# Kernel tuning notes

Measured on AMD Instinct MI355X. Metric: run time of the kernel, lower is better.

The kernel has to match this reference:

```python
import jax, jax.numpy as jnp
import numpy as np

B, S, HID = 1, 2048, 4096
H, HKV, D = 32, 8, 128
GROUPS = H // HKV
ROPE_BASE = 10000.0


def setup_inputs() -> dict:
    key = jax.random.key(0)
    k1, k2, k3, k4, k5 = jax.random.split(key, 5)
    s = 0.02
    return {
        "hidden_states": jax.random.normal(k1, (B, S, HID), dtype=jnp.float32),
        "Wq": jax.random.normal(k2, (H * D, HID), dtype=jnp.float32) * s,
        "Wk": jax.random.normal(k3, (HKV * D, HID), dtype=jnp.float32) * s,
        "Wv": jax.random.normal(k4, (HKV * D, HID), dtype=jnp.float32) * s,
        "Wo": jax.random.normal(k5, (HID, H * D), dtype=jnp.float32) * s,
    }


def _rotate_half(x):
    x1, x2 = x[..., : D // 2], x[..., D // 2 :]
    return jnp.concatenate((-x2, x1), axis=-1)


def _rope_tables(seq_len):
    inv_freq = 1.0 / (ROPE_BASE ** (jnp.arange(0, D, 2, dtype=jnp.float32) / D))
    t = jnp.arange(seq_len, dtype=jnp.float32)
    freqs = jnp.outer(t, inv_freq)            # [S, D/2]
    emb = jnp.concatenate((freqs, freqs), -1)  # [S, D]
    return jnp.cos(emb)[None, None], jnp.sin(emb)[None, None]  # [1,1,S,D]


def reference(hidden_states, Wq, Wk, Wv, Wo):
    b, s, _ = hidden_states.shape
    scale = D ** -0.5
    q = (hidden_states @ Wq.T).reshape(b, s, H, D).transpose(0, 2, 1, 3)    # [B,H,S,D]
    k = (hidden_states @ Wk.T).reshape(b, s, HKV, D).transpose(0, 2, 1, 3)  # [B,HKV,S,D]
    v = (hidden_states @ Wv.T).reshape(b, s, HKV, D).transpose(0, 2, 1, 3)

    cos, sin = _rope_tables(s)
    q = q * cos + _rotate_half(q) * sin
    k = k * cos + _rotate_half(k) * sin

    # repeat_kv: h = kv_h * groups + g -> consecutive repeat along head axis
    k_rep = jnp.repeat(k, GROUPS, axis=1)  # [B,H,S,D]
    v_rep = jnp.repeat(v, GROUPS, axis=1)

    scores = jnp.einsum("bhqd,bhkd->bhqk", q, k_rep) * scale
    causal = jnp.tril(jnp.ones((s, s), dtype=bool))
    scores = jnp.where(causal[None, None], scores, jnp.finfo(scores.dtype).min)
    probs = jax.nn.softmax(scores, axis=-1)
    attn = jnp.einsum("bhqk,bhkd->bhqd", probs, v_rep)  # [B,H,S,D]
    attn = attn.transpose(0, 2, 1, 3).reshape(b, s, H * D)
    return attn @ Wo.T
```

## Files before the change

### kernel.cpp

```cpp
#include <hip/hip_runtime.h>

#define AS1 __attribute__((address_space(1)))
#define AS3 __attribute__((address_space(3)))

typedef __bf16 bf16;
typedef __bf16 bf16x8 __attribute__((ext_vector_type(8)));
typedef float f32x4 __attribute__((ext_vector_type(4)));

__device__ __forceinline__ void gld_lds16(const bf16* g, bf16* l) {
    __builtin_amdgcn_global_load_lds((const AS1 void*)g, (AS3 void*)l, 16, 0, 0);
}

#define SB0 __builtin_amdgcn_sched_barrier(0)
#define BARX do { SB0; __builtin_amdgcn_s_barrier(); SB0; } while (0)

__global__ void cvt_all_kernel(const float4* __restrict__ h, const float4* __restrict__ wq,
                               const float4* __restrict__ wk, const float4* __restrict__ wv,
                               const float4* __restrict__ wo, ushort4* __restrict__ hs,
                               ushort4* __restrict__ wb) {
    const int i = blockIdx.x * 256 + threadIdx.x;
    const float4* src;
    ushort4* dst;
    if (i < 2097152)      { src = h  + i;             dst = hs + i; }
    else if (i < 6291456) { src = wq + (i - 2097152); dst = wb + (i - 2097152); }
    else if (i < 7340032) { src = wk + (i - 6291456); dst = wb + 4194304 + (i - 6291456); }
    else if (i < 8388608) { src = wv + (i - 7340032); dst = wb + 5242880 + (i - 7340032); }
    else                  { src = wo + (i - 8388608); dst = wb + 6291456 + (i - 8388608); }
    const float4 v = *src;
    ushort4 r;
    r.x = __builtin_bit_cast(unsigned short, (bf16)v.x);
    r.y = __builtin_bit_cast(unsigned short, (bf16)v.y);
    r.z = __builtin_bit_cast(unsigned short, (bf16)v.z);
    r.w = __builtin_bit_cast(unsigned short, (bf16)v.w);
    *dst = r;
}

template <bool OUTF32>
__launch_bounds__(512, 2)
__global__ void gemm_8ph_kernel(const bf16* __restrict__ A, const bf16* __restrict__ W,
                                void* __restrict__ Cout, int M, int N, int K) {
    __shared__ __align__(16) bf16 Asl[2][256 * 64];
    __shared__ __align__(16) bf16 Bsl[2][256 * 64];

    const int tn = blockIdx.x * 256;
    const int tm = blockIdx.y * 256;
    const int tid = threadIdx.x;
    const int wave = tid >> 6;
    const int lane = tid & 63;
    const int laneR = lane & 15;
    const int laneS = lane >> 4;
    const int wmB = (wave >> 2) * 128;
    const int wnB = (wave & 3) * 64;
    const int NT = K >> 6;
    const int NI = NT >> 1;

    auto stageA = [&](int t, int h) {
        if (t >= NT) return;
        const int d = t & 1, k0 = t << 6;
#pragma unroll
        for (int iss = 0; iss < 2; ++iss) {
            const int c = iss * 512 + tid;
            const int row = c >> 3, sl = c & 7;
            gld_lds16(A + (size_t)(tm + h * 128 + row) * K + k0 + ((sl ^ (row & 7)) << 3),
                      &Asl[d][h * 8192 + (iss * 512 + wave * 64) * 8]);
        }
    };
    auto stageB = [&](int t, int h) {
        if (t >= NT) return;
        const int d = t & 1, k0 = t << 6;
#pragma unroll
        for (int iss = 0; iss < 2; ++iss) {
            const int c = iss * 512 + tid;
            const int row = c >> 3, sl = c & 7;
            gld_lds16(W + (size_t)(tn + h * 128 + row) * K + k0 + ((sl ^ (row & 7)) << 3),
                      &Bsl[d][h * 8192 + (iss * 512 + wave * 64) * 8]);
        }
    };

    bf16x8 aF[8], bF0[4], bF1[4];
    f32x4 acc[8][4] = {};

#define RD_A(d, mh) do { _Pragma("unroll") for (int m = 0; m < 4; ++m) \
    _Pragma("unroll") for (int ks = 0; ks < 2; ++ks) { \
        const int row_ = wmB + (mh) * 64 + m * 16 + laneR; \
        const int sl_ = (ks * 4 + laneS) ^ (row_ & 7); \
        aF[m * 2 + ks] = *(const bf16x8*)&Asl[d][row_ * 64 + sl_ * 8]; } } while (0)

#define RD_B(d, nh, DST) do { _Pragma("unroll") for (int n = 0; n < 2; ++n) \
    _Pragma("unroll") for (int ks = 0; ks < 2; ++ks) { \
        const int row_ = wnB + (nh) * 32 + n * 16 + laneR; \
        const int sl_ = (ks * 4 + laneS) ^ (row_ & 7); \
        DST[n * 2 + ks] = *(const bf16x8*)&Bsl[d][row_ * 64 + sl_ * 8]; } } while (0)

#define MMAQ(mh, nh, BSRC) do { __builtin_amdgcn_s_setprio(1); \
    _Pragma("unroll") for (int m = 0; m < 4; ++m) \
    _Pragma("unroll") for (int n = 0; n < 2; ++n) \
    _Pragma("unroll") for (int ks = 0; ks < 2; ++ks) \
        acc[(mh) * 4 + m][(nh) * 2 + n] = __builtin_amdgcn_mfma_f32_16x16x32_bf16( \
            aF[m * 2 + ks], BSRC[n * 2 + ks], acc[(mh) * 4 + m][(nh) * 2 + n], 0, 0, 0); \
    __builtin_amdgcn_s_setprio(0); } while (0)

    stageA(0, 0); stageA(0, 1); stageB(0, 0); stageB(0, 1); stageA(1, 0);
    SB0; asm volatile("s_waitcnt vmcnt(2)" ::: "memory"); BARX;

    for (int i = 0; i < NI; ++i) {
        const int u = i * 2;
        const bool last = (i == NI - 1);
        RD_A(0, 0); RD_B(0, 0, bF0); stageA(u + 1, 1);
        BARX; MMAQ(0, 0, bF0); BARX;
        RD_B(0, 1, bF1); stageB(u + 1, 0);
        BARX; MMAQ(0, 1, bF1); BARX;
        RD_A(0, 1); stageB(u + 1, 1);
        BARX; MMAQ(1, 1, bF1); BARX;
        RD_B(0, 0, bF0); stageA(u + 2, 0);
        BARX; MMAQ(1, 0, bF0);
        SB0;
        if (last) asm volatile("s_waitcnt vmcnt(0)" ::: "memory");
        else      asm volatile("s_waitcnt vmcnt(2)" ::: "memory");
        BARX;
        RD_A(1, 0); RD_B(1, 0, bF0); stageA(u + 2, 1);
        BARX; MMAQ(0, 0, bF0); BARX;
        RD_B(1, 1, bF1); stageB(u + 2, 0);
        BARX; MMAQ(0, 1, bF1); BARX;
        RD_A(1, 1); stageB(u + 2, 1);
        BARX; MMAQ(1, 1, bF1); BARX;
        RD_B(1, 0, bF0); stageA(u + 3, 0);
        BARX; MMAQ(1, 0, bF0);
        SB0;
        if (last) asm volatile("s_waitcnt vmcnt(0)" ::: "memory");
        else      asm volatile("s_waitcnt vmcnt(2)" ::: "memory");
        BARX;
    }
#undef RD_A
#undef RD_B
#undef MMAQ

    const int rbase = laneS * 4;
#pragma unroll
    for (int mf = 0; mf < 8; ++mf)
#pragma unroll
        for (int nf = 0; nf < 4; ++nf)
#pragma unroll
            for (int rr = 0; rr < 4; ++rr) {
                const size_t row = (size_t)tm + wmB + mf * 16 + rbase + rr;
                const size_t col = (size_t)tn + wnB + nf * 16 + laneR;
                if constexpr (OUTF32) ((float*)Cout)[row * N + col] = acc[mf][nf][rr];
                else                  ((bf16*)Cout)[row * N + col] = (bf16)acc[mf][nf][rr];
            }
    (void)M;
}

template <int BN, bool OUTF32>
__launch_bounds__(512, 2)
__global__ void gemm8p_kernel(const bf16* __restrict__ A, const bf16* __restrict__ W,
                              void* __restrict__ Cout, int M, int N, int K) {
    constexpr int NF = BN / 64;
    constexpr int IB = BN / 128;
    __shared__ __align__(16) bf16 Asl[4][128 * 32];
    __shared__ __align__(16) bf16 Bsl[4][BN * 32];

    const int tn = blockIdx.x * BN;
    const int tm = blockIdx.y * 128;
    const int tid = threadIdx.x;
    const int wave = tid >> 6;
    const int lane = tid & 63;
    const int laneR = lane & 15;
    const int laneS = lane >> 4;
    const int wmB = (wave >> 2) * 64;
    const int wnB = (wave & 3) * (BN / 4);
    const int NT = K >> 5;
    const int sofs = (laneS ^ ((laneR >> 1) & 3)) << 3;

    auto stage = [&](int t) {
        const int slot = t & 3;
        const int k0 = t << 5;
        {
            const int row = tid >> 2, g = tid & 3;
            const int sg = g ^ ((row >> 1) & 3);
            gld_lds16(A + (size_t)(tm + row) * K + k0 + sg * 8, &Asl[slot][wave * 512]);
        }
#pragma unroll
        for (int i = 0; i < IB; ++i) {
            const int row = i * 128 + (tid >> 2), g = tid & 3;
            const int sg = g ^ ((row >> 1) & 3);
            gld_lds16(W + (size_t)(tn + row) * K + k0 + sg * 8,
                      &Bsl[slot][i * 4096 + wave * 512]);
        }
    };

    f32x4 acc[4][NF] = {};

    stage(0); stage(1); stage(2);
    asm volatile("s_waitcnt vmcnt(6)" ::: "memory");
    SB0;
    __builtin_amdgcn_s_barrier();
    SB0;

    for (int t = 0; t < NT; ++t) {
        const int slot = t & 3;
        bf16x8 af[4], bfr[NF];
#pragma unroll
        for (int mf = 0; mf < 4; ++mf)
            af[mf] = *(const bf16x8*)&Asl[slot][(wmB + mf * 16 + laneR) * 32 + sofs];
#pragma unroll
        for (int nf = 0; nf < NF; ++nf)
            bfr[nf] = *(const bf16x8*)&Bsl[slot][(wnB + nf * 16 + laneR) * 32 + sofs];

        if (t + 3 < NT) stage(t + 3);

#pragma unroll
        for (int mf = 0; mf < 4; ++mf)
#pragma unroll
            for (int nf = 0; nf < NF; ++nf)
                acc[mf][nf] = __builtin_amdgcn_mfma_f32_16x16x32_bf16(af[mf], bfr[nf], acc[mf][nf], 0, 0, 0);

        SB0;
        if (t + 3 < NT)       asm volatile("s_waitcnt vmcnt(6)" ::: "memory");
        else if (t + 3 == NT) asm volatile("s_waitcnt vmcnt(3)" ::: "memory");
        else                  asm volatile("s_waitcnt vmcnt(0)" ::: "memory");
        SB0;
        __builtin_amdgcn_s_barrier();
        SB0;
    }

    const int rbase = laneS * 4;
#pragma unroll
    for (int mf = 0; mf < 4; ++mf)
#pragma unroll
        for (int nf = 0; nf < NF; ++nf)
#pragma unroll
            for (int rr = 0; rr < 4; ++rr) {
                const size_t row = (size_t)tm + wmB + mf * 16 + rbase + rr;
                const size_t col = (size_t)tn + wnB + nf * 16 + laneR;
                if constexpr (OUTF32) ((float*)Cout)[row * N + col] = acc[mf][nf][rr];
                else                  ((bf16*)Cout)[row * N + col] = (bf16)acc[mf][nf][rr];
            }
    (void)M;
}

__global__ void rope_table_kernel(float* __restrict__ ct, float* __restrict__ st) {
    const int idx = blockIdx.x * 256 + threadIdx.x;
    const int f = idx & 63;
    const int s = idx >> 6;
    const float th = s * expf(-0.14391156831212787f * (float)f);
    ct[idx] = cosf(th);
    st[idx] = sinf(th);
}

__global__ void rope_qk_kernel(const bf16* __restrict__ C, bf16* __restrict__ Qr, bf16* __restrict__ Kr,
                               const float* __restrict__ ct, const float* __restrict__ st) {
    const int idx = blockIdx.x * 256 + threadIdx.x;
    const int NQ = 2048 * 32 * 64;
    const float QSC = 0.12751743561884394f;
    if (idx < NQ) {
        const int f = idx & 63;
        const int t = idx >> 6;
        const int h = t & 31;
        const int s = t >> 5;
        const float x1 = (float)C[(size_t)s * 6144 + h * 128 + f];
        const float x2 = (float)C[(size_t)s * 6144 + h * 128 + f + 64];
        const float cs = ct[(s << 6) + f], sn = st[(s << 6) + f];
        bf16* dst = Qr + ((size_t)h * 2048 + s) * 128 + f;
        dst[0]  = (bf16)((x1 * cs - x2 * sn) * QSC);
        dst[64] = (bf16)((x2 * cs + x1 * sn) * QSC);
    } else {
        const int i2 = idx - NQ;
        const int f = i2 & 63;
        const int t = i2 >> 6;
        const int h = t & 7;
        const int s = t >> 3;
        const float x1 = (float)C[(size_t)s * 6144 + 4096 + h * 128 + f];
        const float x2 = (float)C[(size_t)s * 6144 + 4096 + h * 128 + f + 64];
        const float cs = ct[(s << 6) + f], sn = st[(s << 6) + f];
        bf16* dst = Kr + ((size_t)h * 2048 + s) * 128 + f;
        dst[0]  = (bf16)(x1 * cs - x2 * sn);
        dst[64] = (bf16)(x2 * cs + x1 * sn);
    }
}

__global__ void transpose_v_kernel(const bf16* __restrict__ C, bf16* __restrict__ Vt) {
    __shared__ __align__(16) unsigned short t[64][136];
    const int hkv = blockIdx.x >> 5;
    const int st = blockIdx.x & 31;
    const int s0 = st * 64;
    const int tid = threadIdx.x;
#pragma unroll
    for (int it = 0; it < 4; ++it) {
        const int l = it * 2048 + tid * 8;
        const int r = l >> 7, c = l & 127;
        *(bf16x8*)&t[r][c] = *(const bf16x8*)&C[(size_t)(s0 + r) * 6144 + 5120 + hkv * 128 + c];
    }
    __syncthreads();
#pragma unroll
    for (int it = 0; it < 8; ++it) {
        const int o = it * 1024 + tid * 4;
        const int d = o >> 6, j = o & 63;
        ushort4 pk;
        pk.x = t[j + 0][d];
        pk.y = t[j + 1][d];
        pk.z = t[j + 2][d];
        pk.w = t[j + 3][d];
        *(ushort4*)&Vt[((size_t)hkv * 128 + d) * 2048 + s0 + j] = pk;
    }
}

__launch_bounds__(256, 1)
__global__ void flash_attn_kernel(const bf16* __restrict__ Qr, const bf16* __restrict__ Kr,
                                  const bf16* __restrict__ Vt, bf16* __restrict__ Aout) {
    __shared__ __align__(16) bf16 Klds[2][128 * 128];
    __shared__ __align__(16) bf16 Vlds[2][128 * 128];
    __shared__ __align__(16) char Plds[4][4096];

    const int bid = blockIdx.x;
    const int hkv = bid & 7;
    const int r = bid >> 3;
    const int h = hkv * 4 + (r & 3);
    const int pa = r >> 2;
    const int qbA = 15 - pa, qbB = pa;
    const int tid = threadIdx.x;
    const int wave = tid >> 6, lane = tid & 63;
    const int laneR = lane & 15;
    const int laneS = lane >> 4;
    const int laneK = laneS * 8;
    const int rbase = laneS * 4;

    const bf16* Kh = Kr + (size_t)hkv * 2048 * 128;
    const bf16* Vh = Vt + (size_t)hkv * 128 * 2048;
    char* Pw = Plds[wave];

    auto stageK = [&](int kv0, int buf) {
#pragma unroll
        for (int s = 0; s < 8; ++s) {
            const int chunk = wave * 8 + s;
            const int L = chunk * 64 + lane;
            const int row = L >> 4, sl = L & 15;
            gld_lds16(Kh + (size_t)(kv0 + row) * 128 + ((sl ^ (row & 7)) << 3),
                      &Klds[buf][chunk * 512]);
        }
    };
    auto stageV = [&](int kv0, int buf) {
#pragma unroll
        for (int s = 0; s < 8; ++s) {
            const int chunk = wave * 8 + s;
            const int L = chunk * 64 + lane;
            const int row = L >> 4, sl = L & 15;
            gld_lds16(Vh + (size_t)row * 2048 + kv0 + ((sl ^ (row & 7)) << 3),
                      &Vlds[buf][chunk * 512]);
        }
    };

    int qbcur = qbA;
    int q0w = qbA * 128 + wave * 32;
    int tloc = 0;

    bf16x8 qf[2][4];
    auto loadQ = [&]() {
#pragma unroll
        for (int mi = 0; mi < 2; ++mi)
#pragma unroll
            for (int kc = 0; kc < 4; ++kc)
                qf[mi][kc] = *(const bf16x8*)&Qr[((size_t)h * 2048 + q0w + mi * 16 + laneR) * 128 + kc * 32 + laneK];
    };
    loadQ();

    f32x4 o[2][8] = {};
    float mrow[2][4], lrow[2][4];
#pragma unroll
    for (int mi = 0; mi < 2; ++mi)
#pragma unroll
        for (int rr = 0; rr < 4; ++rr) { mrow[mi][rr] = -1e30f; lrow[mi][rr] = 0.f; }

    stageK(0, 0);
    stageV(0, 0);
    __syncthreads();

    for (int g = 0; g < 17; ++g) {
        const int buf = g & 1;
        if (g < 16) {
            const int tn = (g + 1 <= qbA) ? (g + 1) : (g - qbA);
            stageK(tn * 128, buf ^ 1);
            stageV(tn * 128, buf ^ 1);
        }
        const int kv0 = tloc * 128;

        f32x4 sc[2][8] = {};
        __builtin_amdgcn_s_setprio(1);
#pragma unroll
        for (int kc = 0; kc < 4; ++kc) {
            bf16x8 kf[8];
#pragma unroll
            for (int j = 0; j < 8; ++j) {
                const int row = j * 16 + laneR;
                kf[j] = *(const bf16x8*)((const char*)Klds[buf] + row * 256 +
                                         ((kc * 64 + laneS * 16) ^ ((row & 7) << 4)));
            }
#pragma unroll
            for (int mi = 0; mi < 2; ++mi)
#pragma unroll
                for (int j = 0; j < 8; ++j)
                    sc[mi][j] = __builtin_amdgcn_mfma_f32_16x16x32_bf16(qf[mi][kc], kf[j], sc[mi][j], 0, 0, 0);
        }
        __builtin_amdgcn_s_setprio(0);

        if (tloc == qbcur) {
#pragma unroll
            for (int mi = 0; mi < 2; ++mi)
#pragma unroll
                for (int j = 0; j < 8; ++j)
#pragma unroll
                    for (int rr = 0; rr < 4; ++rr) {
                        const int qr = q0w + mi * 16 + rbase + rr;
                        const int kr = kv0 + j * 16 + laneR;
                        if (kr > qr) sc[mi][j][rr] = -1e30f;
                    }
        }

#pragma unroll
        for (int mi = 0; mi < 2; ++mi) {
#pragma unroll
            for (int rr = 0; rr < 4; ++rr) {
                float v = sc[mi][0][rr];
#pragma unroll
                for (int j = 1; j < 8; ++j) v = fmaxf(v, sc[mi][j][rr]);
                v = fmaxf(v, __shfl_xor(v, 1, 64));
                v = fmaxf(v, __shfl_xor(v, 2, 64));
                v = fmaxf(v, __shfl_xor(v, 4, 64));
                v = fmaxf(v, __shfl_xor(v, 8, 64));
                float m0 = mrow[mi][rr];
                if (v - m0 > 8.0f) {
                    const float fac = __builtin_exp2f(m0 - v);
                    mrow[mi][rr] = v;
                    m0 = v;
                    lrow[mi][rr] *= fac;
#pragma unroll
                    for (int j = 0; j < 8; ++j) o[mi][j][rr] *= fac;
                }
                float rs = 0.f;
#pragma unroll
                for (int j = 0; j < 8; ++j) {
                    const float p = __builtin_exp2f(sc[mi][j][rr] - m0);
                    sc[mi][j][rr] = p;
                    rs += p;
                }
                rs += __shfl_xor(rs, 1, 64);
                rs += __shfl_xor(rs, 2, 64);
                rs += __shfl_xor(rs, 4, 64);
                rs += __shfl_xor(rs, 8, 64);
                lrow[mi][rr] += rs;
            }
        }

#pragma unroll
        for (int hf = 0; hf < 2; ++hf) {
#pragma unroll
            for (int mi = 0; mi < 2; ++mi)
#pragma unroll
                for (int j = 0; j < 4; ++j)
#pragma unroll
                    for (int rr = 0; rr < 4; ++rr) {
                        const int row = mi * 16 + rbase + rr;
                        *(bf16*)(Pw + row * 128 + ((j * 32 + laneR * 2) ^ ((row & 7) << 4))) =
                            (bf16)sc[mi][hf * 4 + j][rr];
                    }
            __builtin_amdgcn_s_setprio(1);
#pragma unroll
            for (int kc = 0; kc < 2; ++kc) {
                bf16x8 pf[2];
#pragma unroll
                for (int mi = 0; mi < 2; ++mi) {
                    const int row = mi * 16 + laneR;
                    pf[mi] = *(const bf16x8*)(Pw + row * 128 + ((kc * 64 + laneS * 16) ^ ((row & 7) << 4)));
                }
                const int kcg = hf * 2 + kc;
                bf16x8 vf[8];
#pragma unroll
                for (int j = 0; j < 8; ++j) {
                    const int row = j * 16 + laneR;
                    vf[j] = *(const bf16x8*)((const char*)Vlds[buf] + row * 256 +
                                             ((kcg * 64 + laneS * 16) ^ ((row & 7) << 4)));
                }
#pragma unroll
                for (int mi = 0; mi < 2; ++mi)
#pragma unroll
                    for (int j = 0; j < 8; ++j)
                        o[mi][j] = __builtin_amdgcn_mfma_f32_16x16x32_bf16(pf[mi], vf[j], o[mi][j], 0, 0, 0);
            }
            __builtin_amdgcn_s_setprio(0);
        }

        if (tloc == qbcur) {
#pragma unroll
            for (int mi = 0; mi < 2; ++mi) {
                float rinv[4];
#pragma unroll
                for (int rr = 0; rr < 4; ++rr) rinv[rr] = 1.0f / lrow[mi][rr];
#pragma unroll
                for (int j = 0; j < 8; ++j)
#pragma unroll
                    for (int rr = 0; rr < 4; ++rr) {
                        const size_t row = (size_t)q0w + mi * 16 + rbase + rr;
                        Aout[row * 4096 + h * 128 + j * 16 + laneR] = (bf16)(o[mi][j][rr] * rinv[rr]);
                    }
            }
            if (g < 16) {
                qbcur = qbB;
                q0w = qbB * 128 + wave * 32;
                tloc = 0;
                loadQ();
#pragma unroll
                for (int mi = 0; mi < 2; ++mi)
#pragma unroll
                    for (int rr = 0; rr < 4; ++rr) { mrow[mi][rr] = -1e30f; lrow[mi][rr] = 0.f; }
#pragma unroll
                for (int mi = 0; mi < 2; ++mi)
#pragma unroll
                    for (int j = 0; j < 8; ++j)
                        o[mi][j] = f32x4{0.f, 0.f, 0.f, 0.f};
            }
        } else {
            ++tloc;
        }

        __syncthreads();
    }
}

extern "C" void kernel_launch(void* const* d_in, const int* in_sizes, int n_in,
                              void* d_out, int out_size, void* d_ws, size_t ws_size,
                              hipStream_t stream) {
    const float* hidden = (const float*)d_in[0];
    const float* Wq = (const float*)d_in[1];
    const float* Wk = (const float*)d_in[2];
    const float* Wv = (const float*)d_in[3];
    const float* Wo = (const float*)d_in[4];
    float* out = (float*)d_out;
    char* ws = (char*)d_ws;

    bf16* hs = (bf16*)(ws + 0);
    bf16* Wb = (bf16*)(ws + 16777216);
    bf16* Cq = (bf16*)(ws + 100663296);
    bf16* Qr = (bf16*)(ws + 125829120);
    bf16* Kr = (bf16*)(ws + 142606336);
    bf16* Vt = (bf16*)(ws + 146800640);
    bf16* At = (bf16*)(ws + 150994944);
    float* ct = (float*)(ws + 0);
    float* st = (float*)(ws + 524288);
    (void)ws_size; (void)in_sizes; (void)n_in; (void)out_size;

    cvt_all_kernel<<<49152, 256, 0, stream>>>((const float4*)hidden, (const float4*)Wq,
                                              (const float4*)Wk, (const float4*)Wv,
                                              (const float4*)Wo, (ushort4*)hs, (ushort4*)Wb);

    gemm_8ph_kernel<false><<<dim3(24, 8), 512, 0, stream>>>(hs, Wb, Cq, 2048, 6144, 4096);

    rope_table_kernel<<<512, 256, 0, stream>>>(ct, st);

    rope_qk_kernel<<<20480, 256, 0, stream>>>(Cq, Qr, Kr, ct, st);

    transpose_v_kernel<<<256, 256, 0, stream>>>(Cq, Vt);

    flash_attn_kernel<<<256, 256, 0, stream>>>(Qr, Kr, Vt, At);

    gemm8p_kernel<256, true><<<dim3(16, 16), 512, 0, stream>>>(At, Wb + 25165824, out, 2048, 4096, 4096);
}
```

Before: 351.1 us.

## Restructure flash attention to 64-wide KV tiles, one Q block per CTA, two CTAs/CU

The flash attention kernel moves from 128-wide KV tiles with paired causal Q blocks per CTA to 64-wide KV tiles, one Q block per CTA, and 512 CTAs. Shared memory is halved, with the P buffer aliased into the consumed K buffer, so launch bounds can allow two CTAs per CU. Waves whose rows are fully masked skip compute via a per-wave liveness check. This trades the old triangular load-balancing pairing and adds an extra barrier per tile for better occupancy, and it risks tail imbalance from the uneven per-CTA work.

Measured after the change: 378.8 us. +7.9%, slower.

```diff
diff --git a/kernel.cpp b/kernel.cpp
--- a/kernel.cpp
+++ b/kernel.cpp
@@ -304,64 +304,55 @@
     }
 }
 
-__launch_bounds__(256, 1)
+__launch_bounds__(256, 2)
 __global__ void flash_attn_kernel(const bf16* __restrict__ Qr, const bf16* __restrict__ Kr,
                                   const bf16* __restrict__ Vt, bf16* __restrict__ Aout) {
-    __shared__ __align__(16) bf16 Klds[2][128 * 128];
-    __shared__ __align__(16) bf16 Vlds[2][128 * 128];
-    __shared__ __align__(16) char Plds[4][4096];
+    __shared__ __align__(16) bf16 Klds[2][64 * 128];
+    __shared__ __align__(16) bf16 Vlds[2][128 * 64];
 
     const int bid = blockIdx.x;
     const int hkv = bid & 7;
-    const int r = bid >> 3;
-    const int h = hkv * 4 + (r & 3);
-    const int pa = r >> 2;
-    const int qbA = 15 - pa, qbB = pa;
+    const int hh = (bid >> 3) & 3;
+    const int qb = 15 - (bid >> 5);
+    const int h = hkv * 4 + hh;
     const int tid = threadIdx.x;
     const int wave = tid >> 6, lane = tid & 63;
     const int laneR = lane & 15;
     const int laneS = lane >> 4;
     const int laneK = laneS * 8;
     const int rbase = laneS * 4;
+    const int q0w = qb * 128 + wave * 32;
 
     const bf16* Kh = Kr + (size_t)hkv * 2048 * 128;
     const bf16* Vh = Vt + (size_t)hkv * 128 * 2048;
-    char* Pw = Plds[wave];
 
     auto stageK = [&](int kv0, int buf) {
 #pragma unroll
-        for (int s = 0; s < 8; ++s) {
-            const int chunk = wave * 8 + s;
+        for (int s = 0; s < 4; ++s) {
+            const int chunk = wave * 4 + s;
             const int L = chunk * 64 + lane;
-            const int row = L >> 4, sl = L & 15;
-            gld_lds16(Kh + (size_t)(kv0 + row) * 128 + ((sl ^ (row & 7)) << 3),
+            const int krow = L >> 4, kc16 = L & 15;
+            gld_lds16(Kh + (size_t)(kv0 + krow) * 128 + ((kc16 ^ (krow & 7)) << 3),
                       &Klds[buf][chunk * 512]);
         }
     };
     auto stageV = [&](int kv0, int buf) {
 #pragma unroll
-        for (int s = 0; s < 8; ++s) {
-            const int chunk = wave * 8 + s;
+        for (int s = 0; s < 4; ++s) {
+            const int chunk = wave * 4 + s;
             const int L = chunk * 64 + lane;
-            const int row = L >> 4, sl = L & 15;
-            gld_lds16(Vh + (size_t)row * 2048 + kv0 + ((sl ^ (row & 7)) << 3),
+            const int vrow = L >> 3, vc8 = L & 7;
+            gld_lds16(Vh + (size_t)vrow * 2048 + kv0 + ((vc8 ^ (vrow & 7)) << 3),
                       &Vlds[buf][chunk * 512]);
         }
     };
 
-    int qbcur = qbA;
-    int q0w = qbA * 128 + wave * 32;
-    int tloc = 0;
-
     bf16x8 qf[2][4];
-    auto loadQ = [&]() {
-#pragma unroll
-        for (int mi = 0; mi < 2; ++mi)
-#pragma unroll
-            for (int kc = 0; kc < 4; ++kc)
-                qf[mi][kc] = *(const bf16x8*)&Qr[((size_t)h * 2048 + q0w + mi * 16 + laneR) * 128 + kc * 32 + laneK];
-    };
-    loadQ();
+#pragma unroll
+    for (int mi = 0; mi < 2; ++mi)
+#pragma unroll
+        for (int kc = 0; kc < 4; ++kc)
+            qf[mi][kc] = *(const bf16x8*)&Qr[((size_t)h * 2048 + q0w + mi * 16 + laneR) * 128 + kc * 32 + laneK];
 
     f32x4 o[2][8] = {};
     float mrow[2][4], lrow[2][4];
@@ -370,88 +361,93 @@
 #pragma unroll
         for (int rr = 0; rr < 4; ++rr) { mrow[mi][rr] = -1e30f; lrow[mi][rr] = 0.f; }
 
+    const int ntiles = 2 * qb + 2;
     stageK(0, 0);
     stageV(0, 0);
-    __syncthreads();
-
-    for (int g = 0; g < 17; ++g) {
-        const int buf = g & 1;
-        if (g < 16) {
-            const int tn = (g + 1 <= qbA) ? (g + 1) : (g - qbA);
-            stageK(tn * 128, buf ^ 1);
-            stageV(tn * 128, buf ^ 1);
-        }
-        const int kv0 = tloc * 128;
-
-        f32x4 sc[2][8] = {};
-        __builtin_amdgcn_s_setprio(1);
-#pragma unroll
-        for (int kc = 0; kc < 4; ++kc) {
-            bf16x8 kf[8];
-#pragma unroll
-            for (int j = 0; j < 8; ++j) {
-                const int row = j * 16 + laneR;
-                kf[j] = *(const bf16x8*)((const char*)Klds[buf] + row * 256 +
-                                         ((kc * 64 + laneS * 16) ^ ((row & 7) << 4)));
-            }
-#pragma unroll
-            for (int mi = 0; mi < 2; ++mi)
-#pragma unroll
-                for (int j = 0; j < 8; ++j)
-                    sc[mi][j] = __builtin_amdgcn_mfma_f32_16x16x32_bf16(qf[mi][kc], kf[j], sc[mi][j], 0, 0, 0);
-        }
-        __builtin_amdgcn_s_setprio(0);
-
-        if (tloc == qbcur) {
-#pragma unroll
-            for (int mi = 0; mi < 2; ++mi)
-#pragma unroll
-                for (int j = 0; j < 8; ++j)
-#pragma unroll
-                    for (int rr = 0; rr < 4; ++rr) {
-                        const int qr = q0w + mi * 16 + rbase + rr;
-                        const int kr = kv0 + j * 16 + laneR;
-                        if (kr > qr) sc[mi][j][rr] = -1e30f;
+    SB0; asm volatile("s_waitcnt vmcnt(0)" ::: "memory"); BARX;
+
+    for (int t = 0; t < ntiles; ++t) {
+        const int buf = t & 1;
+        const int kv0 = t * 64;
+        if (t + 1 < ntiles) {
+            stageK(kv0 + 64, buf ^ 1);
+            stageV(kv0 + 64, buf ^ 1);
+        }
+        const bool live = (kv0 <= q0w + 31);
+
+        f32x4 sc[2][4] = {};
+        if (live) {
+            __builtin_amdgcn_s_setprio(1);
+#pragma unroll
+            for (int kc = 0; kc < 4; ++kc) {
+                bf16x8 kf[4];
+#pragma unroll
+                for (int j = 0; j < 4; ++j) {
+                    const int row = j * 16 + laneR;
+                    kf[j] = *(const bf16x8*)((const char*)Klds[buf] + row * 256 +
+                                             ((kc * 64 + laneS * 16) ^ ((row & 7) << 4)));
+                }
+#pragma unroll
+                for (int mi = 0; mi < 2; ++mi)
+#pragma unroll
+                    for (int j = 0; j < 4; ++j)
+                        sc[mi][j] = __builtin_amdgcn_mfma_f32_16x16x32_bf16(qf[mi][kc], kf[j], sc[mi][j], 0, 0, 0);
+            }
+            __builtin_amdgcn_s_setprio(0);
+        }
+
+        BARX;
+
+        if (live) {
+            if (kv0 + 63 > q0w) {
+#pragma unroll
+                for (int mi = 0; mi < 2; ++mi)
+#pragma unroll
+                    for (int j = 0; j < 4; ++j)
+#pragma unroll
+                        for (int rr = 0; rr < 4; ++rr) {
+                            const int qr = q0w + mi * 16 + rbase + rr;
+                            const int kr = kv0 + j * 16 + laneR;
+                            if (kr > qr) sc[mi][j][rr] = -1e30f;
+                        }
+            }
+
+#pragma unroll
+            for (int mi = 0; mi < 2; ++mi) {
+#pragma unroll
+                for (int rr = 0; rr < 4; ++rr) {
+                    float v = sc[mi][0][rr];
+#pragma unroll
+                    for (int j = 1; j < 4; ++j) v = fmaxf(v, sc[mi][j][rr]);
+                    v = fmaxf(v, __shfl_xor(v, 1, 64));
+                    v = fmaxf(v, __shfl_xor(v, 2, 64));
+                    v = fmaxf(v, __shfl_xor(v, 4, 64));
+                    v = fmaxf(v, __shfl_xor(v, 8, 64));
+                    float m0 = mrow[mi][rr];
+                    if (v - m0 > 8.0f) {
+                        const float fac = __builtin_exp2f(m0 - v);
+                        mrow[mi][rr] = v;
+                        m0 = v;
+                        lrow[mi][rr] *= fac;
+#pragma unroll
+                        for (int j = 0; j < 8; ++j) o[mi][j][rr] *= fac;
                     }
-        }
-
-#pragma unroll
-        for (int mi = 0; mi < 2; ++mi) {
-#pragma unroll
-            for (int rr = 0; rr < 4; ++rr) {
-                float v = sc[mi][0][rr];
-#pragma unroll
-                for (int j = 1; j < 8; ++j) v = fmaxf(v, sc[mi][j][rr]);
-                v = fmaxf(v, __shfl_xor(v, 1, 64));
-                v = fmaxf(v, __shfl_xor(v, 2, 64));
-                v = fmaxf(v, __shfl_xor(v, 4, 64));
-                v = fmaxf(v, __shfl_xor(v, 8, 64));
-                float m0 = mrow[mi][rr];
-                if (v - m0 > 8.0f) {
-                    const float fac = __builtin_exp2f(m0 - v);
-                    mrow[mi][rr] = v;
-                    m0 = v;
-                    lrow[mi][rr] *= fac;
-#pragma unroll
-                    for (int j = 0; j < 8; ++j) o[mi][j][rr] *= fac;
+                    float rs = 0.f;
+#pragma unroll
+                    for (int j = 0; j < 4; ++j) {
+                        const float p = __builtin_exp2f(sc[mi][j][rr] - m0);
+                        sc[mi][j][rr] = p;
+                        rs += p;
+                    }
+                    rs += __shfl_xor(rs, 1, 64);
+                    rs += __shfl_xor(rs, 2, 64);
+                    rs += __shfl_xor(rs, 4, 64);
+                    rs += __shfl_xor(rs, 8, 64);
+                    lrow[mi][rr] += rs;
                 }
-                float rs = 0.f;
-#pragma unroll
-                for (int j = 0; j < 8; ++j) {
-                    const float p = __builtin_exp2f(sc[mi][j][rr] - m0);
-                    sc[mi][j][rr] = p;
-                    rs += p;
-                }
-                rs += __shfl_xor(rs, 1, 64);
-                rs += __shfl_xor(rs, 2, 64);
-                rs += __shfl_xor(rs, 4, 64);
-                rs += __shfl_xor(rs, 8, 64);
-                lrow[mi][rr] += rs;
-            }
-        }
-
-#pragma unroll
-        for (int hf = 0; hf < 2; ++hf) {
+            }
+
+            char* Pw = (char*)Klds[buf] + wave * 4096;
 #pragma unroll
             for (int mi = 0; mi < 2; ++mi)
 #pragma unroll
@@ -460,8 +456,9 @@
                     for (int rr = 0; rr < 4; ++rr) {
                         const int row = mi * 16 + rbase + rr;
                         *(bf16*)(Pw + row * 128 + ((j * 32 + laneR * 2) ^ ((row & 7) << 4))) =
-                            (bf16)sc[mi][hf * 4 + j][rr];
+                            (bf16)sc[mi][j][rr];
                     }
+
             __builtin_amdgcn_s_setprio(1);
 #pragma unroll
             for (int kc = 0; kc < 2; ++kc) {
@@ -471,13 +468,12 @@
                     const int row = mi * 16 + laneR;
                     pf[mi] = *(const bf16x8*)(Pw + row * 128 + ((kc * 64 + laneS * 16) ^ ((row & 7) << 4)));
                 }
-                const int kcg = hf * 2 + kc;
                 bf16x8 vf[8];
 #pragma unroll
                 for (int j = 0; j < 8; ++j) {
                     const int row = j * 16 + laneR;
-                    vf[j] = *(const bf16x8*)((const char*)Vlds[buf] + row * 256 +
-                                             ((kcg * 64 + laneS * 16) ^ ((row & 7) << 4)));
+                    vf[j] = *(const bf16x8*)((const char*)Vlds[buf] + row * 128 +
+                                             ((kc * 64 + laneS * 16) ^ ((row & 7) << 4)));
                 }
 #pragma unroll
                 for (int mi = 0; mi < 2; ++mi)
@@ -488,40 +484,21 @@
             __builtin_amdgcn_s_setprio(0);
         }
 
-        if (tloc == qbcur) {
-#pragma unroll
-            for (int mi = 0; mi < 2; ++mi) {
-                float rinv[4];
-#pragma unroll
-                for (int rr = 0; rr < 4; ++rr) rinv[rr] = 1.0f / lrow[mi][rr];
-#pragma unroll
-                for (int j = 0; j < 8; ++j)
-#pragma unroll
-                    for (int rr = 0; rr < 4; ++rr) {
-                        const size_t row = (size_t)q0w + mi * 16 + rbase + rr;
-                        Aout[row * 4096 + h * 128 + j * 16 + laneR] = (bf16)(o[mi][j][rr] * rinv[rr]);
-                    }
-            }
-            if (g < 16) {
-                qbcur = qbB;
-                q0w = qbB * 128 + wave * 32;
-                tloc = 0;
-                loadQ();
-#pragma unroll
-                for (int mi = 0; mi < 2; ++mi)
-#pragma unroll
-                    for (int rr = 0; rr < 4; ++rr) { mrow[mi][rr] = -1e30f; lrow[mi][rr] = 0.f; }
-#pragma unroll
-                for (int mi = 0; mi < 2; ++mi)
-#pragma unroll
-                    for (int j = 0; j < 8; ++j)
-                        o[mi][j] = f32x4{0.f, 0.f, 0.f, 0.f};
-            }
-        } else {
-            ++tloc;
-        }
-
-        __syncthreads();
+        SB0; asm volatile("s_waitcnt vmcnt(0)" ::: "memory"); BARX;
+    }
+
+#pragma unroll
+    for (int mi = 0; mi < 2; ++mi) {
+        float rinv[4];
+#pragma unroll
+        for (int rr = 0; rr < 4; ++rr) rinv[rr] = 1.0f / lrow[mi][rr];
+#pragma unroll
+        for (int j = 0; j < 8; ++j)
+#pragma unroll
+            for (int rr = 0; rr < 4; ++rr) {
+                const size_t row = (size_t)q0w + mi * 16 + rbase + rr;
+                Aout[row * 4096 + h * 128 + j * 16 + laneR] = (bf16)(o[mi][j][rr] * rinv[rr]);
+            }
     }
 }
 
@@ -554,12 +531,11 @@
     gemm_8ph_kernel<false><<<dim3(24, 8), 512, 0, stream>>>(hs, Wb, Cq, 2048, 6144, 4096);
 
     rope_table_kernel<<<512, 256, 0, stream>>>(ct, st);
-
     rope_qk_kernel<<<20480, 256, 0, stream>>>(Cq, Qr, Kr, ct, st);
 
     transpose_v_kernel<<<256, 256, 0, stream>>>(Cq, Vt);
 
-    flash_attn_kernel<<<256, 256, 0, stream>>>(Qr, Kr, Vt, At);
+    flash_attn_kernel<<<512, 256, 0, stream>>>(Qr, Kr, Vt, At);
 
     gemm8p_kernel<256, true><<<dim3(16, 16), 512, 0, stream>>>(At, Wb + 25165824, out, 2048, 4096, 4096);
 }
```
